# Optimization experiments

Measured on AMD Instinct MI355X. Metric: run time of the kernel, lower is better.

Reference implementation:

```python
import jax, jax.numpy as jnp
import numpy as np

NUM_HEADS = 16


def _make_rope(n, half_dim, dtype=jnp.float32):
    # standard rotary frequencies: theta = 10000^{-2i/d}
    inv_freq = 1.0 / (10000.0 ** (np.arange(0, half_dim, dtype=np.float32) / half_dim))
    t = np.arange(n, dtype=np.float32)
    ang = np.outer(t, inv_freq)  # [n, half_dim]
    return jnp.asarray(np.cos(ang), dtype), jnp.asarray(np.sin(ang), dtype)


def setup_inputs() -> dict:
    key = jax.random.key(0)
    ks = jax.random.split(key, 10)
    B, N, C = 2, 2048, 1024
    H = NUM_HEADS
    hd = C // H
    q = jax.random.normal(ks[0], (B, N, C), jnp.float32)
    k = jax.random.normal(ks[1], (B, N, C), jnp.float32)
    v = jax.random.normal(ks[2], (B, N, C), jnp.float32)
    cos, sin = _make_rope(N, hd // 2)
    s = 1.0 / np.sqrt(C)
    Wq = jax.random.normal(ks[3], (C, C), jnp.float32) * s
    bq = jax.random.normal(ks[4], (C,), jnp.float32) * 0.02
    Wk = jax.random.normal(ks[5], (C, C), jnp.float32) * s
    bk = jax.random.normal(ks[6], (C,), jnp.float32) * 0.02
    Wv = jax.random.normal(ks[7], (C, C), jnp.float32) * s
    bv = jax.random.normal(ks[8], (C,), jnp.float32) * 0.02
    return {"q": q, "k": k, "v": v,
            "q_cos": cos, "q_sin": sin, "k_cos": cos, "k_sin": sin,
            "Wq": Wq, "bq": bq, "Wk": Wk, "bk": bk, "Wv": Wv, "bv": bv}


def _rope(x, cos, sin):
    # x: [B, H, N, hd]; pairs (x[...,2j], x[...,2j+1]) form complex numbers,
    # rotated by freqs_cis of shape [N, hd//2] (broadcast over B, H).
    xr = x[..., 0::2]
    xi = x[..., 1::2]
    c = cos[None, None]  # [1,1,N,hd//2]
    s = sin[None, None]
    out_r = xr * c - xi * s
    out_i = xr * s + xi * c
    return jnp.stack([out_r, out_i], axis=-1).reshape(x.shape)


def reference(q, k, v, q_cos, q_sin, k_cos, k_sin, Wq, bq, Wk, bk, Wv, bv):
    B, Nq, C = q.shape
    Nk = k.shape[1]
    H = NUM_HEADS
    hd = C // H
    scale = hd ** -0.5
    # QKV projections (torch nn.Linear: x @ W.T + b), split into heads
    qh = (q @ Wq.T + bq).reshape(B, Nq, H, hd).transpose(0, 2, 1, 3)  # [B,H,Nq,hd]
    kh = (k @ Wk.T + bk).reshape(B, Nk, H, hd).transpose(0, 2, 1, 3)
    vh = (v @ Wv.T + bv).reshape(B, Nk, H, hd).transpose(0, 2, 1, 3)
    # inline RoPE on q and k
    qh = _rope(qh, q_cos, q_sin)
    kh = _rope(kh, k_cos, k_sin)
    # scaled dot-product attention (mask=None, dropout=0, non-causal)
    scores = jnp.einsum('bhqd,bhkd->bhqk', qh, kh) * scale
    attn = jax.nn.softmax(scores, axis=-1)
    out = jnp.einsum('bhqk,bhkd->bhqd', attn, vh)
    # merge heads; NOTE: self.proj is never applied in the original forward
    return out.transpose(0, 2, 1, 3).reshape(B, Nq, C)
```

## Files before the change

kernel.cpp:

```cpp
#include <hip/hip_runtime.h>
#include <hip/hip_bf16.h>

typedef float f32x4 __attribute__((ext_vector_type(4)));
typedef float f32x16 __attribute__((ext_vector_type(16)));
typedef short bf16x8 __attribute__((ext_vector_type(8)));

#define NSEQ 2048
#define CDIM 1024
#define NHEAD 16
#define HDIM 64
#define MROWS 4096
#define QSCALE 0.18033688011f
#define DEFER_THR 11.5416f

__device__ __forceinline__ unsigned short f2bf(float f) {
    unsigned int u = __builtin_bit_cast(unsigned int, f);
    u += 0x7FFFu + ((u >> 16) & 1u);
    return (unsigned short)(u >> 16);
}

__device__ __forceinline__ unsigned pkbf(float lo, float hi_) {
    unsigned r;
    asm("v_cvt_pk_bf16_f32 %0, %1, %2" : "=v"(r) : "v"(lo), "v"(hi_));
    return r;
}

__device__ __forceinline__ void gload16(const void* g, void* l) {
    __builtin_amdgcn_global_load_lds(
        (const __attribute__((address_space(1))) unsigned int*)g,
        (__attribute__((address_space(3))) unsigned int*)l, 16, 0, 0);
}

__global__ __launch_bounds__(256) void cvt6_kernel(
    const float* __restrict__ q, const float* __restrict__ k, const float* __restrict__ v,
    const float* __restrict__ wq, const float* __restrict__ wk, const float* __restrict__ wv,
    unsigned short* __restrict__ dq, unsigned short* __restrict__ dk, unsigned short* __restrict__ dv,
    unsigned short* __restrict__ dwq, unsigned short* __restrict__ dwk, unsigned short* __restrict__ dwv)
{
    int b = blockIdx.x;
    const float* s; unsigned short* d; int base;
    if (b < 4096)       { s = q;  d = dq;  base = b; }
    else if (b < 8192)  { s = k;  d = dk;  base = b - 4096; }
    else if (b < 12288) { s = v;  d = dv;  base = b - 8192; }
    else if (b < 13312) { s = wq; d = dwq; base = b - 12288; }
    else if (b < 14336) { s = wk; d = dwk; base = b - 13312; }
    else                { s = wv; d = dwv; base = b - 14336; }
    int i = (base * 256 + threadIdx.x) * 4;
    float4 t4 = *reinterpret_cast<const float4*>(s + i);
    ushort4 o;
    o.x = f2bf(t4.x); o.y = f2bf(t4.y); o.z = f2bf(t4.z); o.w = f2bf(t4.w);
    *reinterpret_cast<ushort4*>(d + i) = o;
}

__global__ __launch_bounds__(256) void gemm_rope_kernel(
    const unsigned short* __restrict__ Xq, const unsigned short* __restrict__ Xk,
    const unsigned short* __restrict__ Xv,
    const unsigned short* __restrict__ Wqb, const unsigned short* __restrict__ Wkb,
    const unsigned short* __restrict__ Wvb,
    const float* __restrict__ bq, const float* __restrict__ bk, const float* __restrict__ bv,
    const float* __restrict__ qcos, const float* __restrict__ qsin,
    const float* __restrict__ kcos, const float* __restrict__ ksin,
    unsigned short* __restrict__ Qh, unsigned short* __restrict__ Kh,
    unsigned short* __restrict__ VT)
{
    __shared__ unsigned short Al[128][72];
    __shared__ unsigned short Bl[128][72];

    const int tid  = threadIdx.x;
    const int wave = tid >> 6;
    const int lane = tid & 63;
    const int lr   = lane & 15;
    const int lg   = lane >> 4;
    const int lk   = lg * 8;
    const int wm   = wave >> 1;
    const int wn   = wave & 1;
    const int m0   = blockIdx.y * 128;
    const int j0   = blockIdx.x * 128;
    const int z    = blockIdx.z;

    const unsigned short* X = (z == 0) ? Xq : (z == 1) ? Xk : Xv;
    const unsigned short* W = (z == 0) ? Wqb : (z == 1) ? Wkb : Wvb;
    const float* bias = (z == 0) ? bq : (z == 1) ? bk : bv;
    const float* cosb = (z == 0) ? qcos : kcos;
    const float* sinb = (z == 0) ? qsin : ksin;

    f32x4 acc[4][4];
    const f32x4 zero4 = {0.f, 0.f, 0.f, 0.f};
    #pragma unroll
    for (int a = 0; a < 4; a++)
        #pragma unroll
        for (int b = 0; b < 4; b++) acc[a][b] = zero4;

    for (int k0 = 0; k0 < CDIM; k0 += 64) {
        __syncthreads();
        #pragma unroll
        for (int it = 0; it < 4; it++) {
            int c = tid + it * 256;
            int row = c >> 3, col = (c & 7) << 3;
            *reinterpret_cast<bf16x8*>(&Al[row][col]) =
                *reinterpret_cast<const bf16x8*>(X + (size_t)(m0 + row) * CDIM + k0 + col);
            *reinterpret_cast<bf16x8*>(&Bl[row][col]) =
                *reinterpret_cast<const bf16x8*>(W + (size_t)(j0 + row) * CDIM + k0 + col);
        }
        __syncthreads();
        #pragma unroll
        for (int ks = 0; ks < 2; ks++) {
            bf16x8 af[4], bfm[4];
            #pragma unroll
            for (int mi = 0; mi < 4; mi++)
                af[mi] = *reinterpret_cast<const bf16x8*>(&Al[wm * 64 + 16 * mi + lr][ks * 32 + lk]);
            #pragma unroll
            for (int ni = 0; ni < 4; ni++)
                bfm[ni] = *reinterpret_cast<const bf16x8*>(&Bl[wn * 64 + 16 * ni + lr][ks * 32 + lk]);
            #pragma unroll
            for (int mi = 0; mi < 4; mi++)
                #pragma unroll
                for (int ni = 0; ni < 4; ni++)
                    acc[mi][ni] = __builtin_amdgcn_mfma_f32_16x16x32_bf16(
                        af[mi], bfm[ni], acc[mi][ni], 0, 0, 0);
        }
    }

    #pragma unroll
    for (int mi = 0; mi < 4; mi++) {
        const int mbase = m0 + wm * 64 + 16 * mi + 4 * lg;
        #pragma unroll
        for (int ni = 0; ni < 4; ni++) {
            const int j  = j0 + wn * 64 + 16 * ni + lr;
            const float bj = bias[j];
            if (z == 2) {
                const int b = mbase >> 11, n = mbase & 2047;
                const int h = j >> 6, d = j & 63;
                ushort4 pk;
                pk.x = f2bf(acc[mi][ni][0] + bj);
                pk.y = f2bf(acc[mi][ni][1] + bj);
                pk.z = f2bf(acc[mi][ni][2] + bj);
                pk.w = f2bf(acc[mi][ni][3] + bj);
                *reinterpret_cast<ushort4*>(VT + ((size_t)((b * NHEAD + h) * HDIM + d) << 11) + n) = pk;
            } else {
                unsigned short* Out = (z == 0) ? Qh : Kh;
                const float scl = (z == 0) ? QSCALE : 1.0f;
                const int hi = (j & 63) >> 1;
                const float sg = (j & 1) ? 1.f : -1.f;
                float vv[4], pp[4];
                #pragma unroll
                for (int r = 0; r < 4; r++) vv[r] = acc[mi][ni][r] + bj;
                #pragma unroll
                for (int r = 0; r < 4; r++) pp[r] = __shfl_xor(vv[r], 1);
                #pragma unroll
                for (int r = 0; r < 4; r++) {
                    const int m = mbase + r;
                    const int b = m >> 11, n = m & 2047;
                    const float c = cosb[n * 32 + hi];
                    const float s = sinb[n * 32 + hi];
                    const float ov = fmaf(vv[r], c, pp[r] * (sg * s)) * scl;
                    Out[((size_t)((b * NHEAD + (j >> 6)) * NSEQ + n) << 6) + (j & 63)] = f2bf(ov);
                }
            }
        }
    }
}

__global__ __launch_bounds__(256, 2) void attn_kernel(
    const unsigned short* __restrict__ Qh, const unsigned short* __restrict__ Kh,
    const unsigned short* __restrict__ VT, float* __restrict__ out)
{
    __shared__ unsigned char Ksm[2][8192];
    __shared__ unsigned char Vsm[2][8192];

    const int tid  = threadIdx.x;
    const int wave = tid >> 6;
    const int lane = tid & 63;
    const int c    = lane & 31;
    const int hi   = lane >> 5;
    const int bh   = blockIdx.y;
    const int q0w  = blockIdx.x * 128 + wave * 32;
    const int sw   = (c & 7) << 4;

    const unsigned short* Qb = Qh + (size_t)bh * NSEQ * HDIM;
    const char* Kb = (const char*)(Kh + (size_t)bh * NSEQ * HDIM);
    const char* Vb = (const char*)(VT + (size_t)bh * HDIM * NSEQ);

    bf16x8 qf[4];
    #pragma unroll
    for (int s = 0; s < 4; s++)
        qf[s] = *reinterpret_cast<const bf16x8*>(
            Qb + (size_t)(q0w + c) * HDIM + s * 16 + hi * 8);

    const f32x16 z16 = {0,0,0,0,0,0,0,0,0,0,0,0,0,0,0,0};
    f32x16 o0 = z16, o1 = z16;
    float mrun = -1e30f, lrun = 0.f;

    const int sr7 = lane >> 3;
    const int scb = ((lane & 7) * 16) ^ (sr7 << 4);
    const int ch0 = wave * 2;

    auto stage = [&](int buf, int n0) {
        #pragma unroll
        for (int i = 0; i < 2; ++i) {
            const int row = (ch0 + i) * 8 + sr7;
            gload16(Kb + (size_t)(n0 + row) * 128 + scb, &Ksm[buf][(ch0 + i) * 1024]);
            gload16(Vb + (size_t)row * (NSEQ * 2) + (size_t)n0 * 2 + scb,
                    &Vsm[buf][(ch0 + i) * 1024]);
        }
    };

    stage(0, 0);
    __syncthreads();
    int cur = 0;

    for (int t = 0; t < 32; ++t) {
        if (t < 31) stage(cur ^ 1, (t + 1) * 64);

        f32x16 s0 = z16, s1 = z16;
        #pragma unroll
        for (int s = 0; s < 4; s++) {
            const int cb = (32 * s + 16 * hi) ^ sw;
            bf16x8 kf0 = *reinterpret_cast<const bf16x8*>(&Ksm[cur][c * 128 + cb]);
            bf16x8 kf1 = *reinterpret_cast<const bf16x8*>(&Ksm[cur][(32 + c) * 128 + cb]);
            s0 = __builtin_amdgcn_mfma_f32_32x32x16_bf16(kf0, qf[s], s0, 0, 0, 0);
            s1 = __builtin_amdgcn_mfma_f32_32x32x16_bf16(kf1, qf[s], s1, 0, 0, 0);
        }

        float tmx[8];
        #pragma unroll
        for (int i = 0; i < 8; i++)
            tmx[i] = fmaxf(fmaxf(s0[2 * i], s0[2 * i + 1]),
                           fmaxf(s1[2 * i], s1[2 * i + 1]));
        float tm = fmaxf(fmaxf(fmaxf(tmx[0], tmx[1]), fmaxf(tmx[2], tmx[3])),
                         fmaxf(fmaxf(tmx[4], tmx[5]), fmaxf(tmx[6], tmx[7])));
        tm = fmaxf(tm, __shfl_xor(tm, 32));

        if (!__all(tm - mrun <= DEFER_THR)) {
            const float mnew  = fmaxf(mrun, tm);
            const float alpha = exp2f(mrun - mnew);
            mrun = mnew;
            lrun *= alpha;
            #pragma unroll
            for (int r = 0; r < 16; r++) {
                const float ar = __shfl(alpha, (r & 3) + 8 * (r >> 2) + 4 * hi);
                o0[r] *= ar;
                o1[r] *= ar;
            }
        }

        #pragma unroll
        for (int r = 0; r < 16; r++) s0[r] = exp2f(s0[r] - mrun);
        #pragma unroll
        for (int r = 0; r < 16; r++) s1[r] = exp2f(s1[r] - mrun);
        float rsx[8];
        #pragma unroll
        for (int i = 0; i < 8; i++)
            rsx[i] = (s0[2 * i] + s0[2 * i + 1]) + (s1[2 * i] + s1[2 * i + 1]);
        float rs = ((rsx[0] + rsx[1]) + (rsx[2] + rsx[3])) +
                   ((rsx[4] + rsx[5]) + (rsx[6] + rsx[7]));
        rs += __shfl_xor(rs, 32);
        lrun += rs;

        unsigned pw[4][4];
        #pragma unroll
        for (int u = 0; u < 4; u++) {
            const f32x16& sv = (u < 2) ? s0 : s1;
            const int b = (u & 1) * 8;
            unsigned x0 = pkbf(sv[b + 0], sv[b + 1]);
            unsigned y0 = pkbf(sv[b + 4], sv[b + 5]);
            asm("v_permlane32_swap_b32 %0, %1" : "+v"(x0), "+v"(y0));
            unsigned x1 = pkbf(sv[b + 2], sv[b + 3]);
            unsigned y1 = pkbf(sv[b + 6], sv[b + 7]);
            asm("v_permlane32_swap_b32 %0, %1" : "+v"(x1), "+v"(y1));
            pw[u][0] = x0; pw[u][1] = x1; pw[u][2] = y0; pw[u][3] = y1;
        }

        #pragma unroll
        for (int u = 0; u < 4; u++) {
            uint4 w;
            w.x = pw[u][0]; w.y = pw[u][1]; w.z = pw[u][2]; w.w = pw[u][3];
            bf16x8 pa = __builtin_bit_cast(bf16x8, w);
            const int cb = (32 * u + 16 * hi) ^ sw;
            bf16x8 vf0 = *reinterpret_cast<const bf16x8*>(&Vsm[cur][c * 128 + cb]);
            bf16x8 vf1 = *reinterpret_cast<const bf16x8*>(&Vsm[cur][(32 + c) * 128 + cb]);
            o0 = __builtin_amdgcn_mfma_f32_32x32x16_bf16(pa, vf0, o0, 0, 0, 0);
            o1 = __builtin_amdgcn_mfma_f32_32x32x16_bf16(pa, vf1, o1, 0, 0, 0);
        }

        __syncthreads();
        cur ^= 1;
    }

    const int b = bh >> 4, h = bh & 15;
    #pragma unroll
    for (int r = 0; r < 16; r++) {
        const int qrow = (r & 3) + 8 * (r >> 2) + 4 * hi;
        const float li  = __shfl(lrun, qrow);
        const float inv = 1.0f / li;
        const int n = q0w + qrow;
        float* op = out + ((size_t)(b * NSEQ + n) << 10) + h * HDIM + c;
        op[0]  = o0[r] * inv;
        op[32] = o1[r] * inv;
    }
}

extern "C" void kernel_launch(void* const* d_in, const int* in_sizes, int n_in,
                              void* d_out, int out_size, void* d_ws, size_t ws_size,
                              hipStream_t stream) {
    const float* q    = (const float*)d_in[0];
    const float* k    = (const float*)d_in[1];
    const float* v    = (const float*)d_in[2];
    const float* qcos = (const float*)d_in[3];
    const float* qsin = (const float*)d_in[4];
    const float* kcos = (const float*)d_in[5];
    const float* ksin = (const float*)d_in[6];
    const float* Wq   = (const float*)d_in[7];
    const float* bq   = (const float*)d_in[8];
    const float* Wk   = (const float*)d_in[9];
    const float* bk   = (const float*)d_in[10];
    const float* Wv   = (const float*)d_in[11];
    const float* bv   = (const float*)d_in[12];
    float* out = (float*)d_out;

    unsigned short* Xqb = (unsigned short*)d_ws;
    unsigned short* Xkb = Xqb + (size_t)MROWS * CDIM;
    unsigned short* Xvb = Xkb + (size_t)MROWS * CDIM;
    unsigned short* Wqb = Xvb + (size_t)MROWS * CDIM;
    unsigned short* Wkb = Wqb + (size_t)CDIM * CDIM;
    unsigned short* Wvb = Wkb + (size_t)CDIM * CDIM;
    unsigned short* Qhb = Wvb + (size_t)CDIM * CDIM;
    unsigned short* Khb = Qhb + (size_t)MROWS * CDIM;
    unsigned short* VTb = Khb + (size_t)MROWS * CDIM;

    cvt6_kernel<<<15360, 256, 0, stream>>>(q, k, v, Wq, Wk, Wv,
                                           Xqb, Xkb, Xvb, Wqb, Wkb, Wvb);

    dim3 gg(CDIM / 128, MROWS / 128, 3);
    gemm_rope_kernel<<<gg, 256, 0, stream>>>(Xqb, Xkb, Xvb, Wqb, Wkb, Wvb,
                                             bq, bk, bv, qcos, qsin, kcos, ksin,
                                             Qhb, Khb, VTb);

    attn_kernel<<<dim3(NSEQ / 128, 2 * NHEAD), 256, 0, stream>>>(Qhb, Khb, VTb, out);
}
```

Before: 137.6 us.

## Triple-buffer attention K/V tiles and use direct-to-LDS loads in GEMM

```diff
diff --git a/kernel.cpp b/kernel.cpp
--- a/kernel.cpp
+++ b/kernel.cpp
@@ -63,15 +63,14 @@
     unsigned short* __restrict__ Qh, unsigned short* __restrict__ Kh,
     unsigned short* __restrict__ VT)
 {
-    __shared__ unsigned short Al[128][72];
-    __shared__ unsigned short Bl[128][72];
+    __shared__ unsigned short Al[128][64];
+    __shared__ unsigned short Bl[128][64];
 
     const int tid  = threadIdx.x;
     const int wave = tid >> 6;
     const int lane = tid & 63;
     const int lr   = lane & 15;
     const int lg   = lane >> 4;
-    const int lk   = lg * 8;
     const int wm   = wave >> 1;
     const int wn   = wave & 1;
     const int m0   = blockIdx.y * 128;
@@ -84,6 +83,9 @@
     const float* cosb = (z == 0) ? qcos : kcos;
     const float* sinb = (z == 0) ? qsin : ksin;
 
+    const int srow = lane >> 3;
+    const int scol = (lane & 7) * 16;
+
     f32x4 acc[4][4];
     const f32x4 zero4 = {0.f, 0.f, 0.f, 0.f};
     #pragma unroll
@@ -94,13 +96,13 @@
     for (int k0 = 0; k0 < CDIM; k0 += 64) {
         __syncthreads();
         #pragma unroll
-        for (int it = 0; it < 4; it++) {
-            int c = tid + it * 256;
-            int row = c >> 3, col = (c & 7) << 3;
-            *reinterpret_cast<bf16x8*>(&Al[row][col]) =
-                *reinterpret_cast<const bf16x8*>(X + (size_t)(m0 + row) * CDIM + k0 + col);
-            *reinterpret_cast<bf16x8*>(&Bl[row][col]) =
-                *reinterpret_cast<const bf16x8*>(W + (size_t)(j0 + row) * CDIM + k0 + col);
+        for (int i = 0; i < 4; i++) {
+            const int ch  = wave * 4 + i;
+            const int row = ch * 8 + srow;
+            gload16((const char*)X + ((size_t)(m0 + row) * CDIM + k0) * 2 + scol,
+                    (char*)&Al[0][0] + ch * 1024);
+            gload16((const char*)W + ((size_t)(j0 + row) * CDIM + k0) * 2 + scol,
+                    (char*)&Bl[0][0] + ch * 1024);
         }
         __syncthreads();
         #pragma unroll
@@ -108,10 +110,12 @@
             bf16x8 af[4], bfm[4];
             #pragma unroll
             for (int mi = 0; mi < 4; mi++)
-                af[mi] = *reinterpret_cast<const bf16x8*>(&Al[wm * 64 + 16 * mi + lr][ks * 32 + lk]);
+                af[mi] = *reinterpret_cast<const bf16x8*>(
+                    (char*)&Al[0][0] + (wm * 64 + 16 * mi + lr) * 128 + ks * 64 + lg * 16);
             #pragma unroll
             for (int ni = 0; ni < 4; ni++)
-                bfm[ni] = *reinterpret_cast<const bf16x8*>(&Bl[wn * 64 + 16 * ni + lr][ks * 32 + lk]);
+                bfm[ni] = *reinterpret_cast<const bf16x8*>(
+                    (char*)&Bl[0][0] + (wn * 64 + 16 * ni + lr) * 128 + ks * 64 + lg * 16);
             #pragma unroll
             for (int mi = 0; mi < 4; mi++)
                 #pragma unroll
@@ -165,8 +169,8 @@
     const unsigned short* __restrict__ Qh, const unsigned short* __restrict__ Kh,
     const unsigned short* __restrict__ VT, float* __restrict__ out)
 {
-    __shared__ unsigned char Ksm[2][8192];
-    __shared__ unsigned char Vsm[2][8192];
+    __shared__ unsigned char Ksm[3][8192];
+    __shared__ unsigned char Vsm[3][8192];
 
     const int tid  = threadIdx.x;
     const int wave = tid >> 6;
@@ -206,13 +210,23 @@
     };
 
     stage(0, 0);
-    __syncthreads();
-    int cur = 0;
+    stage(1, 64);
 
     for (int t = 0; t < 32; ++t) {
-        if (t < 31) stage(cur ^ 1, (t + 1) * 64);
+        const int cur = t % 3;
+        __builtin_amdgcn_s_barrier();
+        if (t < 30) {
+            stage((t + 2) % 3, (t + 2) * 64);
+            asm volatile("s_waitcnt vmcnt(8)" ::: "memory");
+        } else if (t == 30) {
+            asm volatile("s_waitcnt vmcnt(4)" ::: "memory");
+        } else {
+            asm volatile("s_waitcnt vmcnt(0)" ::: "memory");
+        }
+        __builtin_amdgcn_s_barrier();
 
         f32x16 s0 = z16, s1 = z16;
+        __builtin_amdgcn_s_setprio(1);
         #pragma unroll
         for (int s = 0; s < 4; s++) {
             const int cb = (32 * s + 16 * hi) ^ sw;
@@ -221,6 +235,7 @@
             s0 = __builtin_amdgcn_mfma_f32_32x32x16_bf16(kf0, qf[s], s0, 0, 0, 0);
             s1 = __builtin_amdgcn_mfma_f32_32x32x16_bf16(kf1, qf[s], s1, 0, 0, 0);
         }
+        __builtin_amdgcn_s_setprio(0);
 
         float tmx[8];
         #pragma unroll
@@ -271,6 +286,7 @@
             pw[u][0] = x0; pw[u][1] = x1; pw[u][2] = y0; pw[u][3] = y1;
         }
 
+        __builtin_amdgcn_s_setprio(1);
         #pragma unroll
         for (int u = 0; u < 4; u++) {
             uint4 w;
@@ -282,9 +298,7 @@
             o0 = __builtin_amdgcn_mfma_f32_32x32x16_bf16(pa, vf0, o0, 0, 0, 0);
             o1 = __builtin_amdgcn_mfma_f32_32x32x16_bf16(pa, vf1, o1, 0, 0, 0);
         }
-
-        __syncthreads();
-        cur ^= 1;
+        __builtin_amdgcn_s_setprio(0);
     }
 
     const int b = bh >> 4, h = bh & 15;
```

Measured after the change: 145.7 us. 1.06x slower.

## Split attention KV range in two halves with a separate combine kernel

Applied to the files above, without the earlier changes.

```diff
diff --git a/kernel.cpp b/kernel.cpp
--- a/kernel.cpp
+++ b/kernel.cpp
@@ -163,7 +163,8 @@
 
 __global__ __launch_bounds__(256, 2) void attn_kernel(
     const unsigned short* __restrict__ Qh, const unsigned short* __restrict__ Kh,
-    const unsigned short* __restrict__ VT, float* __restrict__ out)
+    const unsigned short* __restrict__ VT, float* __restrict__ out,
+    float* __restrict__ O2, float2* __restrict__ ML)
 {
     __shared__ unsigned char Ksm[2][8192];
     __shared__ unsigned char Vsm[2][8192];
@@ -173,8 +174,10 @@
     const int lane = tid & 63;
     const int c    = lane & 31;
     const int hi   = lane >> 5;
-    const int bh   = blockIdx.y;
-    const int q0w  = blockIdx.x * 128 + wave * 32;
+    const int bh   = blockIdx.x;
+    const int q0w  = blockIdx.y * 128 + wave * 32;
+    const int half = blockIdx.z;
+    const int kbase = half * 1024;
     const int sw   = (c & 7) << 4;
 
     const unsigned short* Qb = Qh + (size_t)bh * NSEQ * HDIM;
@@ -205,14 +208,15 @@
         }
     };
 
-    stage(0, 0);
+    stage(0, kbase);
     __syncthreads();
     int cur = 0;
 
-    for (int t = 0; t < 32; ++t) {
-        if (t < 31) stage(cur ^ 1, (t + 1) * 64);
+    for (int t = 0; t < 16; ++t) {
+        if (t < 15) stage(cur ^ 1, kbase + (t + 1) * 64);
 
         f32x16 s0 = z16, s1 = z16;
+        __builtin_amdgcn_s_setprio(1);
         #pragma unroll
         for (int s = 0; s < 4; s++) {
             const int cb = (32 * s + 16 * hi) ^ sw;
@@ -221,6 +225,7 @@
             s0 = __builtin_amdgcn_mfma_f32_32x32x16_bf16(kf0, qf[s], s0, 0, 0, 0);
             s1 = __builtin_amdgcn_mfma_f32_32x32x16_bf16(kf1, qf[s], s1, 0, 0, 0);
         }
+        __builtin_amdgcn_s_setprio(0);
 
         float tmx[8];
         #pragma unroll
@@ -271,6 +276,7 @@
             pw[u][0] = x0; pw[u][1] = x1; pw[u][2] = y0; pw[u][3] = y1;
         }
 
+        __builtin_amdgcn_s_setprio(1);
         #pragma unroll
         for (int u = 0; u < 4; u++) {
             uint4 w;
@@ -282,22 +288,54 @@
             o0 = __builtin_amdgcn_mfma_f32_32x32x16_bf16(pa, vf0, o0, 0, 0, 0);
             o1 = __builtin_amdgcn_mfma_f32_32x32x16_bf16(pa, vf1, o1, 0, 0, 0);
         }
+        __builtin_amdgcn_s_setprio(0);
 
         __syncthreads();
         cur ^= 1;
     }
 
+    float* obase = half ? O2 : out;
     const int b = bh >> 4, h = bh & 15;
     #pragma unroll
     for (int r = 0; r < 16; r++) {
         const int qrow = (r & 3) + 8 * (r >> 2) + 4 * hi;
-        const float li  = __shfl(lrun, qrow);
-        const float inv = 1.0f / li;
         const int n = q0w + qrow;
-        float* op = out + ((size_t)(b * NSEQ + n) << 10) + h * HDIM + c;
-        op[0]  = o0[r] * inv;
-        op[32] = o1[r] * inv;
+        float* op = obase + ((size_t)(b * NSEQ + n) << 10) + h * HDIM + c;
+        op[0]  = o0[r];
+        op[32] = o1[r];
     }
+    if (hi == 0)
+        ML[((size_t)half * 32 + bh) * NSEQ + q0w + c] = make_float2(mrun, lrun);
+}
+
+__global__ __launch_bounds__(256) void attn_combine(
+    float* __restrict__ out, const float* __restrict__ O2,
+    const float2* __restrict__ ML)
+{
+    const int idx4 = blockIdx.x * 256 + threadIdx.x;
+    const int e    = idx4 * 4;
+    const int row  = e >> 10;
+    const int col  = e & 1023;
+    const int h    = col >> 6;
+    const int b    = row >> 11;
+    const int n    = row & 2047;
+    const int bh   = b * NHEAD + h;
+
+    const float2 ml1 = ML[(size_t)bh * NSEQ + n];
+    const float2 ml2 = ML[((size_t)32 + bh) * NSEQ + n];
+    const float M  = fmaxf(ml1.x, ml2.x);
+    const float w1 = exp2f(ml1.x - M);
+    const float w2 = exp2f(ml2.x - M);
+    const float inv = 1.0f / (w1 * ml1.y + w2 * ml2.y);
+
+    float4 a = reinterpret_cast<float4*>(out)[idx4];
+    float4 d = reinterpret_cast<const float4*>(O2)[idx4];
+    float4 r;
+    r.x = (w1 * a.x + w2 * d.x) * inv;
+    r.y = (w1 * a.y + w2 * d.y) * inv;
+    r.z = (w1 * a.z + w2 * d.z) * inv;
+    r.w = (w1 * a.w + w2 * d.w) * inv;
+    reinterpret_cast<float4*>(out)[idx4] = r;
 }
 
 extern "C" void kernel_launch(void* const* d_in, const int* in_sizes, int n_in,
@@ -328,6 +366,9 @@
     unsigned short* Khb = Qhb + (size_t)MROWS * CDIM;
     unsigned short* VTb = Khb + (size_t)MROWS * CDIM;
 
+    float*  O2 = (float*)Xqb;
+    float2* ML = (float2*)((char*)d_ws + (size_t)16 * 1024 * 1024);
+
     cvt6_kernel<<<15360, 256, 0, stream>>>(q, k, v, Wq, Wk, Wv,
                                            Xqb, Xkb, Xvb, Wqb, Wkb, Wvb);
 
@@ -336,5 +377,8 @@
                                              bq, bk, bv, qcos, qsin, kcos, ksin,
                                              Qhb, Khb, VTb);
 
-    attn_kernel<<<dim3(NSEQ / 128, 2 * NHEAD), 256, 0, stream>>>(Qhb, Khb, VTb, out);
-}
+    attn_kernel<<<dim3(2 * NHEAD, NSEQ / 128, 2), 256, 0, stream>>>(
+        Qhb, Khb, VTb, out, O2, ML);
+
+    attn_combine<<<(MROWS * CDIM / 4) / 256, 256, 0, stream>>>(out, O2, ML);
+}
```

Measured after the change: 143.4 us. +4.3%, slower.
